# Kernel optimization log

Hardware: AMD Instinct MI355X
Metric: run time of the kernel (lower is better)

The kernel has to match this reference:

```python
import jax, jax.numpy as jnp
import numpy as np

B, S, D, O = 1024, 200, 512, 512


def setup_inputs() -> dict:
    key = jax.random.key(0)
    ks = jax.random.split(key, 8)
    x = jax.random.normal(ks[0], (B, S, D), dtype=jnp.float32)
    # prefix mask: sqlen in [2, S] so keys slice [:sqlen-1] is non-empty
    sqlen = jax.random.randint(ks[1], (B,), 2, S + 1)
    mask = (jnp.arange(S)[None, :] < sqlen[:, None]).astype(jnp.int32)
    lim = 1.0 / np.sqrt(D)
    Wq_w = jax.random.uniform(ks[2], (O, D), minval=-lim, maxval=lim)
    Wk_w = jax.random.uniform(ks[3], (O, D), minval=-lim, maxval=lim)
    Wv_w = jax.random.uniform(ks[4], (O, D), minval=-lim, maxval=lim)
    Wq_b = jax.random.uniform(ks[5], (O,), minval=-lim, maxval=lim)
    Wk_b = jax.random.uniform(ks[6], (O,), minval=-lim, maxval=lim)
    Wv_b = jax.random.uniform(ks[7], (O,), minval=-lim, maxval=lim)
    return {"input": x, "mask": mask, "Wq_w": Wq_w, "Wq_b": Wq_b,
            "Wk_w": Wk_w, "Wk_b": Wk_b, "Wv_w": Wv_w, "Wv_b": Wv_b}


def reference(input, mask, Wq_w, Wq_b, Wk_w, Wk_b, Wv_w, Wv_b):
    b, s, d = input.shape
    sqlen = jnp.sum(mask, axis=1).astype(jnp.int32)          # [B]
    # query = last valid token; keys/values = tokens [0, sqlen-1)
    last = input[jnp.arange(b), sqlen - 1]                   # [B, D]
    q = last @ Wq_w.T + Wq_b                                 # [B, O]
    K = jnp.einsum('bsd,od->bso', input, Wk_w) + Wk_b        # [B, S, O]
    V = jnp.einsum('bsd,od->bso', input, Wv_w) + Wv_b        # [B, S, O]
    scores = jnp.einsum('bo,bso->bs', q, K)                  # no 1/sqrt(d), faithful
    valid = jnp.arange(s)[None, :] < (sqlen - 1)[:, None]    # [B, S]
    scores = jnp.where(valid, scores, -jnp.inf)
    attn = jax.nn.softmax(scores, axis=-1)
    out = jnp.einsum('bs,bso->bo', attn, V)                  # [B, O]
    # dropout p=0.5 treated as identity (eval mode / deterministic reference)
    return jnp.tanh(out)
```

## Files before the change

### kernel.cpp

```cpp
#include <hip/hip_runtime.h>
#include <hip/hip_bf16.h>
#include <math.h>

#define B_  1024
#define S_  200
#define D_  512
#define O_  512

__global__ __launch_bounds__(64) void prep_kernel(
    const float* __restrict__ x, const int* __restrict__ mask,
    int* __restrict__ sqlen, float* __restrict__ last)
{
    const int b = blockIdx.x;
    const int lane = threadIdx.x;

    int ssum = 0;
    for (int i = lane; i < S_; i += 64) ssum += mask[b * S_ + i];
#pragma unroll
    for (int off = 32; off; off >>= 1) ssum += __shfl_xor(ssum, off);
    if (lane == 0) sqlen[b] = ssum;

    const float* row = x + ((size_t)b * S_ + (ssum - 1)) * D_;
    float4 v0 = *(const float4*)(row + lane * 8);
    float4 v1 = *(const float4*)(row + lane * 8 + 4);
    *(float4*)(last + (size_t)b * D_ + lane * 8)     = v0;
    *(float4*)(last + (size_t)b * D_ + lane * 8 + 4) = v1;
}

template<bool TB, bool BIAS, bool TANH>
__global__ __launch_bounds__(256) void gemm_kernel(
    const float* __restrict__ A, const float* __restrict__ Bm,
    const float* __restrict__ bias, float* __restrict__ C,
    int M, int N, int K)
{
    constexpr int BM = 64, BN = 64, BK = 16;
    __shared__ float As[BK][BM + 4];
    __shared__ float Bs[BK][BN + 4];

    const int tid = threadIdx.x;
    const int tx = tid & 15;
    const int ty = tid >> 4;
    const int m0 = blockIdx.x * BM;
    const int n0 = blockIdx.y * BN;

    const int ar = tid >> 2;
    const int ac = (tid & 3) << 2;

    float acc[4][4] = {};

    for (int k0 = 0; k0 < K; k0 += BK) {
        float4 av = *(const float4*)(A + (size_t)(m0 + ar) * K + k0 + ac);
        float4 bv;
        if (TB) {
            bv = *(const float4*)(Bm + (size_t)(n0 + ar) * K + k0 + ac);
        } else {
            bv = *(const float4*)(Bm + (size_t)(k0 + (tid >> 4)) * N + n0 + ((tid & 15) << 2));
        }
        __syncthreads();
        As[ac + 0][ar] = av.x; As[ac + 1][ar] = av.y;
        As[ac + 2][ar] = av.z; As[ac + 3][ar] = av.w;
        if (TB) {
            Bs[ac + 0][ar] = bv.x; Bs[ac + 1][ar] = bv.y;
            Bs[ac + 2][ar] = bv.z; Bs[ac + 3][ar] = bv.w;
        } else {
            *(float4*)&Bs[tid >> 4][(tid & 15) << 2] = bv;
        }
        __syncthreads();

#pragma unroll
        for (int kk = 0; kk < BK; ++kk) {
            float4 a4 = *(const float4*)&As[kk][ty << 2];
            float4 b4 = *(const float4*)&Bs[kk][tx << 2];
            float aa[4] = {a4.x, a4.y, a4.z, a4.w};
            float bb[4] = {b4.x, b4.y, b4.z, b4.w};
#pragma unroll
            for (int i = 0; i < 4; ++i)
#pragma unroll
                for (int j = 0; j < 4; ++j)
                    acc[i][j] = fmaf(aa[i], bb[j], acc[i][j]);
        }
    }

#pragma unroll
    for (int i = 0; i < 4; ++i) {
        float o[4];
#pragma unroll
        for (int j = 0; j < 4; ++j) {
            float v = acc[i][j];
            if (BIAS) v += bias[n0 + (tx << 2) + j];
            if (TANH) v = tanhf(v);
            o[j] = v;
        }
        float4 ov = make_float4(o[0], o[1], o[2], o[3]);
        *(float4*)(C + (size_t)(m0 + (ty << 2) + i) * N + n0 + (tx << 2)) = ov;
    }
}

__global__ __launch_bounds__(256) void attn_kernel(
    const float* __restrict__ x, const float* __restrict__ qk,
    const int* __restrict__ sqlen, float* __restrict__ ctx)
{
    const int b    = blockIdx.x;
    const int tid  = threadIdx.x;
    const int wave = tid >> 6;
    const int lane = tid & 63;
    const int L    = sqlen[b] - 1;

    const float* qkb = qk + (size_t)b * D_ + lane * 8;
    const float4 q0 = *(const float4*)qkb;
    const float4 q1 = *(const float4*)(qkb + 4);

    float m = -INFINITY, l = 0.f;
    float acc[8] = {0.f, 0.f, 0.f, 0.f, 0.f, 0.f, 0.f, 0.f};

    int s = wave;
    if (s < L) {
        const float* base = x + (size_t)b * S_ * D_ + lane * 8;
        float4 c0 = *(const float4*)(base + (size_t)s * D_);
        float4 c1 = *(const float4*)(base + (size_t)s * D_ + 4);
        for (;;) {
            const int  sn   = s + 4;
            const bool more = sn < L;
            const int  sp   = more ? sn : s;
            float4 n0 = *(const float4*)(base + (size_t)sp * D_);
            float4 n1 = *(const float4*)(base + (size_t)sp * D_ + 4);

            float p = c0.x * q0.x + c0.y * q0.y + c0.z * q0.z + c0.w * q0.w
                    + c1.x * q1.x + c1.y * q1.y + c1.z * q1.z + c1.w * q1.w;
#pragma unroll
            for (int off = 32; off; off >>= 1) p += __shfl_xor(p, off);

            const float mn = fmaxf(m, p);
            const float r  = __expf(m - mn);
            const float e  = __expf(p - mn);
            l = l * r + e;
            acc[0] = acc[0] * r + e * c0.x;
            acc[1] = acc[1] * r + e * c0.y;
            acc[2] = acc[2] * r + e * c0.z;
            acc[3] = acc[3] * r + e * c0.w;
            acc[4] = acc[4] * r + e * c1.x;
            acc[5] = acc[5] * r + e * c1.y;
            acc[6] = acc[6] * r + e * c1.z;
            acc[7] = acc[7] * r + e * c1.w;
            m = mn;

            if (!more) break;
            s = sn; c0 = n0; c1 = n1;
        }
    }

    __shared__ float s_m[4], s_l[4];
    __shared__ float s_ctx[4][D_];
    if (lane == 0) { s_m[wave] = m; s_l[wave] = l; }
#pragma unroll
    for (int j = 0; j < 8; ++j) s_ctx[wave][lane * 8 + j] = acc[j];
    __syncthreads();

    const float M4 = fmaxf(fmaxf(s_m[0], s_m[1]), fmaxf(s_m[2], s_m[3]));
    const float sc0 = __expf(s_m[0] - M4);
    const float sc1 = __expf(s_m[1] - M4);
    const float sc2 = __expf(s_m[2] - M4);
    const float sc3 = __expf(s_m[3] - M4);
    const float lt  = s_l[0] * sc0 + s_l[1] * sc1 + s_l[2] * sc2 + s_l[3] * sc3;
    const float inv = 1.f / lt;

    const int d = tid * 2;
    float v0 = (s_ctx[0][d]     * sc0 + s_ctx[1][d]     * sc1 +
                s_ctx[2][d]     * sc2 + s_ctx[3][d]     * sc3) * inv;
    float v1 = (s_ctx[0][d + 1] * sc0 + s_ctx[1][d + 1] * sc1 +
                s_ctx[2][d + 1] * sc2 + s_ctx[3][d + 1] * sc3) * inv;
    float2 ov = make_float2(v0, v1);
    *(float2*)(ctx + (size_t)b * D_ + d) = ov;
}

extern "C" void kernel_launch(void* const* d_in, const int* in_sizes, int n_in,
                              void* d_out, int out_size, void* d_ws, size_t ws_size,
                              hipStream_t stream)
{
    const float* x    = (const float*)d_in[0];
    const int*   mask = (const int*)  d_in[1];
    const float* Wq_w = (const float*)d_in[2];
    const float* Wq_b = (const float*)d_in[3];
    const float* Wk_w = (const float*)d_in[4];
    const float* Wk_b = (const float*)d_in[5];
    const float* Wv_w = (const float*)d_in[6];
    const float* Wv_b = (const float*)d_in[7];
    (void)Wk_b; (void)in_sizes; (void)n_in; (void)out_size; (void)ws_size;
    float* out = (float*)d_out;

    char* ws = (char*)d_ws;
    int*   sqlen = (int*)ws;
    float* buf0  = (float*)(ws + 4096);
    float* buf1  = (float*)(ws + 4096 + (1u << 21));

    float* last = buf0;
    float* q    = buf1;
    float* qk   = buf0;
    float* ctx  = buf1;

    prep_kernel<<<B_, 64, 0, stream>>>(x, mask, sqlen, last);

    dim3 g(B_ / 64, O_ / 64);
    gemm_kernel<true,  true,  false><<<g, 256, 0, stream>>>(last, Wq_w, Wq_b, q,  B_, O_, D_);
    gemm_kernel<false, false, false><<<g, 256, 0, stream>>>(q,    Wk_w, nullptr, qk, B_, D_, O_);
    attn_kernel<<<B_, 256, 0, stream>>>(x, qk, sqlen, ctx);
    gemm_kernel<true,  true,  true ><<<g, 256, 0, stream>>>(ctx,  Wv_w, Wv_b, out, B_, O_, D_);
}
```

Before: 613.3 us.

## Fold Wq and Wk into one matrix, retile GEMMs, unroll attention by two tokens

The query and key projections are algebraically folded: a per-call GEMM computes Wq^T·Wk and the folded bias vector Wq_b·Wk, so only one batch-sized GEMM is needed to produce the key-space query. The generic 64x64 GEMM is replaced by a 16x16-tile, single-wave kernel with transpose-mode templates, giving many more small blocks. The attention loop now processes two tokens per wave per iteration, with double-buffered loads, to raise memory-level parallelism. The smaller GEMM tiles reduce data reuse, and the folded weight GEMM adds its own cost.

```diff
diff --git a/kernel.cpp b/kernel.cpp
--- a/kernel.cpp
+++ b/kernel.cpp
@@ -18,6 +18,7 @@
     for (int i = lane; i < S_; i += 64) ssum += mask[b * S_ + i];
 #pragma unroll
     for (int off = 32; off; off >>= 1) ssum += __shfl_xor(ssum, off);
+
     if (lane == 0) sqlen[b] = ssum;
 
     const float* row = x + ((size_t)b * S_ + (ssum - 1)) * D_;
@@ -27,73 +28,101 @@
     *(float4*)(last + (size_t)b * D_ + lane * 8 + 4) = v1;
 }
 
-template<bool TB, bool BIAS, bool TANH>
-__global__ __launch_bounds__(256) void gemm_kernel(
+template<int AMODE, int BMODE, bool BIASOUT, bool BIAS, bool TANH>
+__global__ __launch_bounds__(64) void gemm16(
     const float* __restrict__ A, const float* __restrict__ Bm,
     const float* __restrict__ bias, float* __restrict__ C,
-    int M, int N, int K)
-{
-    constexpr int BM = 64, BN = 64, BK = 16;
-    __shared__ float As[BK][BM + 4];
-    __shared__ float Bs[BK][BN + 4];
-
-    const int tid = threadIdx.x;
-    const int tx = tid & 15;
-    const int ty = tid >> 4;
-    const int m0 = blockIdx.x * BM;
-    const int n0 = blockIdx.y * BN;
-
-    const int ar = tid >> 2;
-    const int ac = (tid & 3) << 2;
-
-    float acc[4][4] = {};
-
-    for (int k0 = 0; k0 < K; k0 += BK) {
-        float4 av = *(const float4*)(A + (size_t)(m0 + ar) * K + k0 + ac);
-        float4 bv;
-        if (TB) {
-            bv = *(const float4*)(Bm + (size_t)(n0 + ar) * K + k0 + ac);
-        } else {
-            bv = *(const float4*)(Bm + (size_t)(k0 + (tid >> 4)) * N + n0 + ((tid & 15) << 2));
-        }
+    float* __restrict__ cvec, const float* __restrict__ bfold,
+    int M, int N, int K, int lda, int ldb)
+{
+    constexpr int SA = (AMODE == 0) ? 22 : 20;
+    constexpr int SB = (BMODE == 0) ? 22 : 20;
+    __shared__ float As[32 * SA];
+    __shared__ float Bs[32 * SB];
+    __shared__ float sBq[32];
+
+    const int lane = threadIdx.x;
+    const int m0 = blockIdx.x * 16;
+    const int n0 = blockIdx.y * 16;
+    const int ly = lane >> 3;
+    const int lx = lane & 7;
+
+    float a00 = 0.f, a01 = 0.f, a10 = 0.f, a11 = 0.f;
+    float cb0 = 0.f, cb1 = 0.f;
+
+    for (int k0 = 0; k0 < K; k0 += 32) {
+        float4 av0, av1, bv0, bv1;
+        if (AMODE == 0) {
+            const float* p = A + (size_t)(m0 + (lane >> 2)) * lda + k0 + ((lane & 3) << 3);
+            av0 = *(const float4*)p;  av1 = *(const float4*)(p + 4);
+        } else {
+            const float* p = A + (size_t)(k0 + (lane >> 1)) * lda + m0 + ((lane & 1) << 3);
+            av0 = *(const float4*)p;  av1 = *(const float4*)(p + 4);
+        }
+        if (BMODE == 0) {
+            const float* p = Bm + (size_t)(n0 + (lane >> 2)) * ldb + k0 + ((lane & 3) << 3);
+            bv0 = *(const float4*)p;  bv1 = *(const float4*)(p + 4);
+        } else {
+            const float* p = Bm + (size_t)(k0 + (lane >> 1)) * ldb + n0 + ((lane & 1) << 3);
+            bv0 = *(const float4*)p;  bv1 = *(const float4*)(p + 4);
+        }
+        float bqv = 0.f;
+        if (BIASOUT) bqv = bfold[k0 + (lane & 31)];
+
         __syncthreads();
-        As[ac + 0][ar] = av.x; As[ac + 1][ar] = av.y;
-        As[ac + 2][ar] = av.z; As[ac + 3][ar] = av.w;
-        if (TB) {
-            Bs[ac + 0][ar] = bv.x; Bs[ac + 1][ar] = bv.y;
-            Bs[ac + 2][ar] = bv.z; Bs[ac + 3][ar] = bv.w;
-        } else {
-            *(float4*)&Bs[tid >> 4][(tid & 15) << 2] = bv;
-        }
+
+        if (AMODE == 0) {
+            const int mr = lane >> 2, kc = (lane & 3) << 3;
+            As[(kc + 0) * SA + mr] = av0.x; As[(kc + 1) * SA + mr] = av0.y;
+            As[(kc + 2) * SA + mr] = av0.z; As[(kc + 3) * SA + mr] = av0.w;
+            As[(kc + 4) * SA + mr] = av1.x; As[(kc + 5) * SA + mr] = av1.y;
+            As[(kc + 6) * SA + mr] = av1.z; As[(kc + 7) * SA + mr] = av1.w;
+        } else {
+            const int kr = lane >> 1, mc = (lane & 1) << 3;
+            *(float4*)&As[kr * SA + mc]     = av0;
+            *(float4*)&As[kr * SA + mc + 4] = av1;
+        }
+        if (BMODE == 0) {
+            const int nr = lane >> 2, kc = (lane & 3) << 3;
+            Bs[(kc + 0) * SB + nr] = bv0.x; Bs[(kc + 1) * SB + nr] = bv0.y;
+            Bs[(kc + 2) * SB + nr] = bv0.z; Bs[(kc + 3) * SB + nr] = bv0.w;
+            Bs[(kc + 4) * SB + nr] = bv1.x; Bs[(kc + 5) * SB + nr] = bv1.y;
+            Bs[(kc + 6) * SB + nr] = bv1.z; Bs[(kc + 7) * SB + nr] = bv1.w;
+        } else {
+            const int kr = lane >> 1, nc = (lane & 1) << 3;
+            *(float4*)&Bs[kr * SB + nc]     = bv0;
+            *(float4*)&Bs[kr * SB + nc + 4] = bv1;
+        }
+        if (BIASOUT && lane < 32) sBq[lane] = bqv;
+
         __syncthreads();
 
 #pragma unroll
-        for (int kk = 0; kk < BK; ++kk) {
-            float4 a4 = *(const float4*)&As[kk][ty << 2];
-            float4 b4 = *(const float4*)&Bs[kk][tx << 2];
-            float aa[4] = {a4.x, a4.y, a4.z, a4.w};
-            float bb[4] = {b4.x, b4.y, b4.z, b4.w};
-#pragma unroll
-            for (int i = 0; i < 4; ++i)
-#pragma unroll
-                for (int j = 0; j < 4; ++j)
-                    acc[i][j] = fmaf(aa[i], bb[j], acc[i][j]);
+        for (int kk = 0; kk < 32; ++kk) {
+            float2 a = *(const float2*)&As[kk * SA + (ly << 1)];
+            float2 b = *(const float2*)&Bs[kk * SB + (lx << 1)];
+            a00 = fmaf(a.x, b.x, a00); a01 = fmaf(a.x, b.y, a01);
+            a10 = fmaf(a.y, b.x, a10); a11 = fmaf(a.y, b.y, a11);
+            if (BIASOUT) {
+                float qv = sBq[kk];
+                cb0 = fmaf(qv, b.x, cb0); cb1 = fmaf(qv, b.y, cb1);
+            }
         }
     }
 
-#pragma unroll
-    for (int i = 0; i < 4; ++i) {
-        float o[4];
-#pragma unroll
-        for (int j = 0; j < 4; ++j) {
-            float v = acc[i][j];
-            if (BIAS) v += bias[n0 + (tx << 2) + j];
-            if (TANH) v = tanhf(v);
-            o[j] = v;
-        }
-        float4 ov = make_float4(o[0], o[1], o[2], o[3]);
-        *(float4*)(C + (size_t)(m0 + (ty << 2) + i) * N + n0 + (tx << 2)) = ov;
+    const int r0 = m0 + (ly << 1);
+    const int c0 = n0 + (lx << 1);
+    float o00 = a00, o01 = a01, o10 = a10, o11 = a11;
+    if (BIAS) {
+        float b0 = bias[c0], b1 = bias[c0 + 1];
+        o00 += b0; o01 += b1; o10 += b0; o11 += b1;
     }
+    if (TANH) { o00 = tanhf(o00); o01 = tanhf(o01); o10 = tanhf(o10); o11 = tanhf(o11); }
+    *(float2*)(C + (size_t)r0 * N + c0)       = make_float2(o00, o01);
+    *(float2*)(C + (size_t)(r0 + 1) * N + c0) = make_float2(o10, o11);
+
+    if (BIASOUT && blockIdx.x == 0 && ly == 0)
+        *(float2*)(cvec + c0) = make_float2(cb0, cb1);
 }
 
 __global__ __launch_bounds__(256) void attn_kernel(
@@ -102,7 +131,7 @@
 {
     const int b    = blockIdx.x;
     const int tid  = threadIdx.x;
-    const int wave = tid >> 6;
+    const int w    = tid >> 6;
     const int lane = tid & 63;
     const int L    = sqlen[b] - 1;
 
@@ -113,47 +142,60 @@
     float m = -INFINITY, l = 0.f;
     float acc[8] = {0.f, 0.f, 0.f, 0.f, 0.f, 0.f, 0.f, 0.f};
 
-    int s = wave;
-    if (s < L) {
+    int s0 = w * 2;
+    if (s0 < L) {
         const float* base = x + (size_t)b * S_ * D_ + lane * 8;
-        float4 c0 = *(const float4*)(base + (size_t)s * D_);
-        float4 c1 = *(const float4*)(base + (size_t)s * D_ + 4);
+        const int s1c = (s0 + 1 < L) ? s0 + 1 : s0;
+        float4 c0 = *(const float4*)(base + (size_t)s0  * D_);
+        float4 c1 = *(const float4*)(base + (size_t)s0  * D_ + 4);
+        float4 c2 = *(const float4*)(base + (size_t)s1c * D_);
+        float4 c3 = *(const float4*)(base + (size_t)s1c * D_ + 4);
         for (;;) {
-            const int  sn   = s + 4;
+            const int  sn   = s0 + 8;
             const bool more = sn < L;
-            const int  sp   = more ? sn : s;
-            float4 n0 = *(const float4*)(base + (size_t)sp * D_);
-            float4 n1 = *(const float4*)(base + (size_t)sp * D_ + 4);
-
-            float p = c0.x * q0.x + c0.y * q0.y + c0.z * q0.z + c0.w * q0.w
-                    + c1.x * q1.x + c1.y * q1.y + c1.z * q1.z + c1.w * q1.w;
-#pragma unroll
-            for (int off = 32; off; off >>= 1) p += __shfl_xor(p, off);
-
-            const float mn = fmaxf(m, p);
-            const float r  = __expf(m - mn);
-            const float e  = __expf(p - mn);
-            l = l * r + e;
-            acc[0] = acc[0] * r + e * c0.x;
-            acc[1] = acc[1] * r + e * c0.y;
-            acc[2] = acc[2] * r + e * c0.z;
-            acc[3] = acc[3] * r + e * c0.w;
-            acc[4] = acc[4] * r + e * c1.x;
-            acc[5] = acc[5] * r + e * c1.y;
-            acc[6] = acc[6] * r + e * c1.z;
-            acc[7] = acc[7] * r + e * c1.w;
+            const int  sp0  = more ? sn : s0;
+            const int  sp1  = (sn + 1 < L) ? sn + 1 : sp0;
+            float4 n0 = *(const float4*)(base + (size_t)sp0 * D_);
+            float4 n1 = *(const float4*)(base + (size_t)sp0 * D_ + 4);
+            float4 n2 = *(const float4*)(base + (size_t)sp1 * D_);
+            float4 n3 = *(const float4*)(base + (size_t)sp1 * D_ + 4);
+
+            float p0 = c0.x*q0.x + c0.y*q0.y + c0.z*q0.z + c0.w*q0.w
+                     + c1.x*q1.x + c1.y*q1.y + c1.z*q1.z + c1.w*q1.w;
+            float p1 = c2.x*q0.x + c2.y*q0.y + c2.z*q0.z + c2.w*q0.w
+                     + c3.x*q1.x + c3.y*q1.y + c3.z*q1.z + c3.w*q1.w;
+#pragma unroll
+            for (int off = 32; off; off >>= 1) {
+                p0 += __shfl_xor(p0, off);
+                p1 += __shfl_xor(p1, off);
+            }
+            if (s0 + 1 >= L) p1 = -INFINITY;
+
+            const float mn = fmaxf(m, fmaxf(p0, p1));
+            const float r  = __expf(m  - mn);
+            const float e0 = __expf(p0 - mn);
+            const float e1 = __expf(p1 - mn);
+            l = l * r + e0 + e1;
+            acc[0] = acc[0]*r + e0*c0.x + e1*c2.x;
+            acc[1] = acc[1]*r + e0*c0.y + e1*c2.y;
+            acc[2] = acc[2]*r + e0*c0.z + e1*c2.z;
+            acc[3] = acc[3]*r + e0*c0.w + e1*c2.w;
+            acc[4] = acc[4]*r + e0*c1.x + e1*c3.x;
+            acc[5] = acc[5]*r + e0*c1.y + e1*c3.y;
+            acc[6] = acc[6]*r + e0*c1.z + e1*c3.z;
+            acc[7] = acc[7]*r + e0*c1.w + e1*c3.w;
             m = mn;
 
             if (!more) break;
-            s = sn; c0 = n0; c1 = n1;
+            s0 = sn; c0 = n0; c1 = n1; c2 = n2; c3 = n3;
         }
     }
 
     __shared__ float s_m[4], s_l[4];
     __shared__ float s_ctx[4][D_];
-    if (lane == 0) { s_m[wave] = m; s_l[wave] = l; }
-#pragma unroll
-    for (int j = 0; j < 8; ++j) s_ctx[wave][lane * 8 + j] = acc[j];
+    if (lane == 0) { s_m[w] = m; s_l[w] = l; }
+#pragma unroll
+    for (int j = 0; j < 8; ++j) s_ctx[w][lane * 8 + j] = acc[j];
     __syncthreads();
 
     const float M4 = fmaxf(fmaxf(s_m[0], s_m[1]), fmaxf(s_m[2], s_m[3]));
@@ -161,7 +203,7 @@
     const float sc1 = __expf(s_m[1] - M4);
     const float sc2 = __expf(s_m[2] - M4);
     const float sc3 = __expf(s_m[3] - M4);
-    const float lt  = s_l[0] * sc0 + s_l[1] * sc1 + s_l[2] * sc2 + s_l[3] * sc3;
+    const float lt  = s_l[0]*sc0 + s_l[1]*sc1 + s_l[2]*sc2 + s_l[3]*sc3;
     const float inv = 1.f / lt;
 
     const int d = tid * 2;
@@ -169,8 +211,7 @@
                 s_ctx[2][d]     * sc2 + s_ctx[3][d]     * sc3) * inv;
     float v1 = (s_ctx[0][d + 1] * sc0 + s_ctx[1][d + 1] * sc1 +
                 s_ctx[2][d + 1] * sc2 + s_ctx[3][d + 1] * sc3) * inv;
-    float2 ov = make_float2(v0, v1);
-    *(float2*)(ctx + (size_t)b * D_ + d) = ov;
+    *(float2*)(ctx + (size_t)b * D_ + d) = make_float2(v0, v1);
 }
 
 extern "C" void kernel_launch(void* const* d_in, const int* in_sizes, int n_in,
@@ -190,19 +231,22 @@
 
     char* ws = (char*)d_ws;
     int*   sqlen = (int*)ws;
-    float* buf0  = (float*)(ws + 4096);
-    float* buf1  = (float*)(ws + 4096 + (1u << 21));
-
-    float* last = buf0;
-    float* q    = buf1;
-    float* qk   = buf0;
-    float* ctx  = buf1;
+    float* cvec  = (float*)(ws + 4096);
+    float* Wqk   = (float*)(ws + 8192);
+    float* last  = (float*)(ws + 8192 + (1u << 20));
+    float* qk    = last + (size_t)B_ * D_;
+    float* ctxb  = qk   + (size_t)B_ * D_;
+
+    gemm16<1, 1, true, false, false><<<dim3(32, 32), 64, 0, stream>>>(
+        Wq_w, Wk_w, nullptr, Wqk, cvec, Wq_b, D_, D_, O_, D_, D_);
 
     prep_kernel<<<B_, 64, 0, stream>>>(x, mask, sqlen, last);
 
-    dim3 g(B_ / 64, O_ / 64);
-    gemm_kernel<true,  true,  false><<<g, 256, 0, stream>>>(last, Wq_w, Wq_b, q,  B_, O_, D_);
-    gemm_kernel<false, false, false><<<g, 256, 0, stream>>>(q,    Wk_w, nullptr, qk, B_, D_, O_);
-    attn_kernel<<<B_, 256, 0, stream>>>(x, qk, sqlen, ctx);
-    gemm_kernel<true,  true,  true ><<<g, 256, 0, stream>>>(ctx,  Wv_w, Wv_b, out, B_, O_, D_);
-}
+    gemm16<0, 1, false, true, false><<<dim3(B_ / 16, D_ / 16), 64, 0, stream>>>(
+        last, Wqk, cvec, qk, nullptr, nullptr, B_, D_, D_, D_, D_);
+
+    attn_kernel<<<B_, 256, 0, stream>>>(x, qk, sqlen, ctxb);
+
+    gemm16<0, 0, false, true, true><<<dim3(B_ / 16, O_ / 16), 64, 0, stream>>>(
+        ctxb, Wv_w, Wv_b, out, nullptr, nullptr, B_, O_, D_, D_, D_);
+}
```

Measured after the change: 592.4 us. 3.4% less time.
